# Performance work log

Hardware: AMD Instinct MI355X
Metric: run time of the kernel (lower is better)

The kernel has to match this reference:

```python
import jax, jax.numpy as jnp
import numpy as np

N_HEADS = 16
ROPE_BASE = 10000.0


def _rope_tables(T, head_dim, dtype):
    inv_freq = 1.0 / (ROPE_BASE ** (jnp.arange(0, head_dim, 2, dtype=jnp.float32) / head_dim))
    t = jnp.arange(T, dtype=jnp.float32)
    freqs = jnp.outer(t, inv_freq)              # (T, head_dim/2)
    emb = jnp.concatenate([freqs, freqs], -1)   # (T, head_dim)
    return jnp.cos(emb).astype(dtype), jnp.sin(emb).astype(dtype)


def _rotate_half(x):
    x1, x2 = jnp.split(x, 2, axis=-1)
    return jnp.concatenate([-x2, x1], axis=-1)


def setup_inputs() -> dict:
    key = jax.random.key(0)
    k1, k2, k3 = jax.random.split(key, 3)
    B, T, C = 2, 2048, 2048
    x = jax.random.normal(k1, (B, T, C), dtype=jnp.float32)
    Wqkv = jax.random.normal(k2, (C, 3 * C), dtype=jnp.float32) * (1.0 / np.sqrt(C))
    Wproj = jax.random.normal(k3, (C, C), dtype=jnp.float32) * (1.0 / np.sqrt(C))
    return {"x": x, "Wqkv": Wqkv, "Wproj": Wproj}


def reference(x, Wqkv, Wproj):
    B, T, C = x.shape
    H = N_HEADS
    D = C // H
    qkv = jnp.einsum('btc,cd->btd', x, Wqkv)            # (B,T,3C)
    q, k, v = jnp.split(qkv, 3, axis=-1)
    # (B,T,C) -> (B,H,T,D)
    q = q.reshape(B, T, H, D).transpose(0, 2, 1, 3)
    k = k.reshape(B, T, H, D).transpose(0, 2, 1, 3)
    v = v.reshape(B, T, H, D).transpose(0, 2, 1, 3)
    cos, sin = _rope_tables(T, D, x.dtype)              # (T,D) each
    q = q * cos + _rotate_half(q) * sin
    k = k * cos + _rotate_half(k) * sin
    scale = 1.0 / jnp.sqrt(jnp.asarray(D, x.dtype))
    att = jnp.einsum('bhqd,bhkd->bhqk', q, k) * scale   # (B,H,T,T)
    causal = jnp.tril(jnp.ones((T, T), dtype=bool))
    att = jnp.where(causal, att, jnp.asarray(-jnp.inf, att.dtype))
    att = jax.nn.softmax(att, axis=-1)
    y = jnp.einsum('bhqk,bhkd->bhqd', att, v)           # (B,H,T,D)
    y = y.transpose(0, 2, 1, 3).reshape(B, T, C)
    return jnp.einsum('btc,cd->btd', y, Wproj)
```

## Files before the change

kernel.cpp:

```cpp
#include <hip/hip_runtime.h>
#include <stdint.h>

#define T_SEQ 2048
#define NH 16
#define HD 128
#define CC 2048
#define N3 6144
#define MM 4096

typedef short bf16x8 __attribute__((ext_vector_type(8)));
typedef float f32x4 __attribute__((ext_vector_type(4)));

__device__ __forceinline__ unsigned short f2bf(float f) {
  unsigned int u = __float_as_uint(f);
  u += 0x7FFF + ((u >> 16) & 1);
  return (unsigned short)(u >> 16);
}
__device__ __forceinline__ float bf2f(unsigned short h) {
  return __uint_as_float(((unsigned int)h) << 16);
}

__global__ __launch_bounds__(256) void k_transpose_cvt(const float* __restrict__ in,
                                                       unsigned short* __restrict__ out,
                                                       int K, int N) {
  __shared__ float tile[32][33];
  int k0 = blockIdx.x * 32;
  int n0 = blockIdx.y * 32;
  int tx = threadIdx.x & 31, ty = threadIdx.x >> 5;
  #pragma unroll
  for (int r = ty; r < 32; r += 8)
    tile[r][tx] = in[(size_t)(k0 + r) * N + n0 + tx];
  __syncthreads();
  #pragma unroll
  for (int r = ty; r < 32; r += 8)
    out[(size_t)(n0 + r) * K + k0 + tx] = f2bf(tile[tx][r]);
}

__global__ __launch_bounds__(256) void k_cvt(const float* __restrict__ in,
                                             unsigned short* __restrict__ out, int n4) {
  int i = blockIdx.x * 256 + threadIdx.x;
  if (i >= n4) return;
  float4 v = ((const float4*)in)[i];
  ushort4 o;
  o.x = f2bf(v.x); o.y = f2bf(v.y); o.z = f2bf(v.z); o.w = f2bf(v.w);
  ((ushort4*)out)[i] = o;
}

template<int NJ, int EPI, int MMAJ>
__global__ __launch_bounds__(512, 1) void k_gemm8(const unsigned short* __restrict__ A,
                                                  const unsigned short* __restrict__ Bt,
                                                  float* __restrict__ C,
                                                  unsigned short* __restrict__ qo,
                                                  unsigned short* __restrict__ ko,
                                                  unsigned short* __restrict__ vo,
                                                  int M, int N, int K) {
  constexpr int BU = NJ / 2;
  constexpr int DSTRIDE = (1 + BU) * 16384;
  extern __shared__ __align__(16) char lds[];
  const int tid = threadIdx.x;
  const int lane = tid & 63;
  const int lr = lane & 15, lg = lane >> 4;
  const int wave = tid >> 6;
  const int wm = wave >> 2, wn = wave & 3;
  const int nwg = gridDim.x;
  const int bid = blockIdx.x;
  const int wg = (bid & 7) * (nwg >> 3) + (bid >> 3);
  const int GX = M >> 7;
  const int GN = N / (NJ * 64);
  const int mt = MMAJ ? (wg % GX) : (wg / GN);
  const int nt = MMAJ ? (wg / GX) : (wg % GN);
  const int m0 = mt * 128, n0 = nt * NJ * 64;
  const int NT = K >> 6;

  auto STAGE = [&](int d, int op, int h, int t) {
    const unsigned short* src = op ? Bt : A;
    const int r0 = (op ? n0 + h * 128 : m0);
    const int kc = t * 64;
    char* base = lds + d * DSTRIDE + op * 16384 + h * 16384;
    #pragma unroll
    for (int l = 0; l < 2; ++l) {
      int p = (l * 512 + tid) * 16;
      int qq = p ^ (((p >> 7) & 7) << 4);
      const unsigned short* g = src + (size_t)(r0 + (qq >> 7)) * K + kc + ((qq & 127) >> 1);
      __builtin_amdgcn_global_load_lds(
          (const __attribute__((address_space(1))) void*)g,
          (__attribute__((address_space(3))) void*)(base + (l * 512 + (tid & 448)) * 16),
          16, 0, 0);
    }
  };
  auto RD = [&](int d, int op, int row, int kb) -> bf16x8 {
    const char* base = lds + d * DSTRIDE + op * 16384;
    int p = row * 128 + kb;
    p ^= ((p >> 7) & 7) << 4;
    return *(const bf16x8*)(base + p);
  };

  f32x4 acc[4][NJ];
  #pragma unroll
  for (int i = 0; i < 4; ++i)
    #pragma unroll
    for (int j = 0; j < NJ; ++j) acc[i][j] = (f32x4){0.f, 0.f, 0.f, 0.f};

  bf16x8 bfrg[NJ][2];

#define PHASE(D, MI, READB, DOST, SD, SO, SH, ST, VM)                                    \
  {                                                                                      \
    if (READB) {                                                                         \
      _Pragma("unroll")                                                                  \
      for (int nj = 0; nj < NJ; ++nj)                                                    \
        _Pragma("unroll")                                                                \
        for (int ks = 0; ks < 2; ++ks)                                                   \
          bfrg[nj][ks] = RD(D, 1, wn * NJ * 16 + nj * 16 + lr, ks * 64 + lg * 16);       \
    }                                                                                    \
    bf16x8 af[2];                                                                        \
    _Pragma("unroll")                                                                    \
    for (int ks = 0; ks < 2; ++ks)                                                       \
      af[ks] = RD(D, 0, wm * 64 + (MI) * 16 + lr, ks * 64 + lg * 16);                    \
    if (DOST) STAGE(SD, SO, SH, ST);                                                     \
    __builtin_amdgcn_s_barrier();                                                        \
    asm volatile("s_waitcnt lgkmcnt(0)" ::: "memory");                                   \
    __builtin_amdgcn_s_setprio(1);                                                       \
    _Pragma("unroll")                                                                    \
    for (int nj = 0; nj < NJ; ++nj)                                                      \
      _Pragma("unroll")                                                                  \
      for (int ks = 0; ks < 2; ++ks)                                                     \
        acc[MI][nj] = __builtin_amdgcn_mfma_f32_16x16x32_bf16(af[ks], bfrg[nj][ks], acc[MI][nj], 0, 0, 0); \
    __builtin_amdgcn_s_setprio(0);                                                       \
    if ((VM) == 6) asm volatile("s_waitcnt vmcnt(6)" ::: "memory");                      \
    if ((VM) == 4) asm volatile("s_waitcnt vmcnt(4)" ::: "memory");                      \
    __builtin_amdgcn_s_barrier();                                                        \
  }

  const int t1 = NT > 1 ? 1 : 0;
  #pragma unroll
  for (int h = 0; h < BU; ++h) STAGE(0, 1, h, 0);
  STAGE(0, 0, 0, 0);
  #pragma unroll
  for (int h = 0; h < BU; ++h) STAGE(1, 1, h, t1);
  if (NJ == 6) asm volatile("s_waitcnt vmcnt(6)" ::: "memory");
  else         asm volatile("s_waitcnt vmcnt(4)" ::: "memory");
  __builtin_amdgcn_s_barrier();

  for (int it = 0; it < (NT >> 1); ++it) {
    const int tb  = 2 * it + 1;
    const int ta1 = min(2 * it + 2, NT - 1);
    const int tb1 = min(2 * it + 3, NT - 1);
    if (NJ == 6) {
      PHASE(0, 0, true,  true, 1, 0, 0, tb,  -1)
      PHASE(0, 1, false, true, 0, 1, 0, ta1, -1)
      PHASE(0, 2, false, true, 0, 1, 1, ta1, -1)
      PHASE(0, 3, false, true, 0, 1, 2, ta1,  6)
      PHASE(1, 0, true,  true, 0, 0, 0, ta1, -1)
      PHASE(1, 1, false, true, 1, 1, 0, tb1, -1)
      PHASE(1, 2, false, true, 1, 1, 1, tb1, -1)
      PHASE(1, 3, false, true, 1, 1, 2, tb1,  6)
    } else {
      PHASE(0, 0, true,  true,  1, 0, 0, tb,  -1)
      PHASE(0, 1, false, true,  0, 1, 0, ta1, -1)
      PHASE(0, 2, false, true,  0, 1, 1, ta1, -1)
      PHASE(0, 3, false, false, 0, 0, 0, 0,    4)
      PHASE(1, 0, true,  true,  0, 0, 0, ta1, -1)
      PHASE(1, 1, false, true,  1, 1, 0, tb1, -1)
      PHASE(1, 2, false, true,  1, 1, 1, tb1, -1)
      PHASE(1, 3, false, false, 0, 0, 0, 0,    4)
    }
  }
#undef PHASE

  #pragma unroll
  for (int mi = 0; mi < 4; ++mi) {
    #pragma unroll
    for (int nj = 0; nj < NJ; ++nj) {
      #pragma unroll
      for (int j = 0; j < 4; ++j) {
        int m = m0 + wm * 64 + mi * 16 + lg * 4 + j;
        int n = n0 + wn * NJ * 16 + nj * 16 + lr;
        float val = acc[mi][nj][j];
        if (EPI == 0) {
          C[(size_t)m * N + n] = val;
        } else {
          int which = n >> 11, cc = n & 2047;
          int h = cc >> 7, d = cc & 127;
          int b = m >> 11, t = m & 2047;
          unsigned short* dst = which == 0 ? qo : (which == 1 ? ko : vo);
          dst[(((size_t)(b * NH + h)) * T_SEQ + t) * HD + d] = f2bf(val);
        }
      }
    }
  }
}

__global__ __launch_bounds__(256) void k_rope(unsigned short* __restrict__ q,
                                              unsigned short* __restrict__ k) {
  int i = blockIdx.x * 256 + threadIdx.x;
  int d = i & 63;
  int t = (i >> 6) & (T_SEQ - 1);
  int bh = i >> 17;
  float invf = exp2f((float)(-2 * d) * (13.287712379549449f / 128.f));
  float ang = (float)t * invf;
  float c = cosf(ang), s = sinf(ang);
  size_t base = ((size_t)bh * T_SEQ + t) * HD + d;
  const float scale = 0.08838834764831845f;
  float q1 = bf2f(q[base]), q2 = bf2f(q[base + 64]);
  q[base]      = f2bf((q1 * c - q2 * s) * scale);
  q[base + 64] = f2bf((q2 * c + q1 * s) * scale);
  float k1 = bf2f(k[base]), k2 = bf2f(k[base + 64]);
  k[base]      = f2bf(k1 * c - k2 * s);
  k[base + 64] = f2bf(k2 * c + k1 * s);
}

__global__ __launch_bounds__(256) void k_transpose_v(const unsigned short* __restrict__ in,
                                                     unsigned short* __restrict__ out) {
  __shared__ unsigned short tile[32][33];
  int bh = blockIdx.z;
  int t0 = blockIdx.x * 32, d0 = blockIdx.y * 32;
  int tx = threadIdx.x & 31, ty = threadIdx.x >> 5;
  const unsigned short* src = in + (size_t)bh * T_SEQ * HD;
  unsigned short* dst = out + (size_t)bh * HD * T_SEQ;
  #pragma unroll
  for (int r = ty; r < 32; r += 8)
    tile[r][tx] = src[(size_t)(t0 + r) * HD + d0 + tx];
  __syncthreads();
  #pragma unroll
  for (int r = ty; r < 32; r += 8)
    dst[(size_t)(d0 + r) * T_SEQ + t0 + tx] = tile[tx][r];
}

__global__ __launch_bounds__(512) void k_attn(const unsigned short* __restrict__ Q,
                                              const unsigned short* __restrict__ K,
                                              const unsigned short* __restrict__ Vt,
                                              unsigned short* __restrict__ Y) {
  __shared__ __align__(16) unsigned short Ks[64 * 128];
  __shared__ __align__(16) unsigned short Vs[128 * 64];
  __shared__ __align__(16) unsigned short Ps[128 * 80];
  const int id = blockIdx.x;
  const int sub = id & 255;
  const int bh = sub & 31;
  const int qtl = (id < 256) ? (15 - (sub >> 5)) : (sub >> 5);
  const int b = bh >> 4, h = bh & 15;
  const int tid = threadIdx.x, wave = tid >> 6, lane = tid & 63;
  const int lr = lane & 15, lg = lane >> 4;
  const int q0 = qtl * 128;
  const int jtmax = 2 * qtl + 1;
  const unsigned short* Qb = Q + (size_t)bh * T_SEQ * HD;
  const unsigned short* Kb = K + (size_t)bh * T_SEQ * HD;
  const unsigned short* Vb = Vt + (size_t)bh * HD * T_SEQ;

  int rkA[2], okA[2], rvA[2], ovA[2], bkA[2], bvA[2];
  #pragma unroll
  for (int it = 0; it < 2; ++it) {
    int c = it * 512 + tid;
    rkA[it] = c >> 4; okA[it] = (c & 15) * 8;
    bkA[it] = (rkA[it] * 256 + (c & 15) * 16) ^ ((rkA[it] & 7) << 4);
    rvA[it] = c >> 3; ovA[it] = (c & 7) * 8;
    bvA[it] = (rvA[it] * 128 + (c & 7) * 16) ^ ((rvA[it] & 7) << 4);
  }

  bf16x8 qf[4];
  #pragma unroll
  for (int kk = 0; kk < 4; ++kk)
    qf[kk] = *(const bf16x8*)(Qb + (size_t)(q0 + wave * 16 + lr) * HD + kk * 32 + lg * 8);

  const f32x4 fzero = {0.f, 0.f, 0.f, 0.f};
  f32x4 oacc[8];
  #pragma unroll
  for (int nd = 0; nd < 8; ++nd) oacc[nd] = fzero;
  float mrow[4], lrow[4];
  #pragma unroll
  for (int j = 0; j < 4; ++j) { mrow[j] = -1e30f; lrow[j] = 0.f; }

  bf16x8 kst[2], vst[2];
  #pragma unroll
  for (int it = 0; it < 2; ++it) {
    kst[it] = *(const bf16x8*)(Kb + (size_t)rkA[it] * HD + okA[it]);
    vst[it] = *(const bf16x8*)(Vb + (size_t)rvA[it] * T_SEQ + ovA[it]);
  }

  for (int jt = 0; jt <= jtmax; ++jt) {
    const int tk0 = jt * 64;
    __syncthreads();
    #pragma unroll
    for (int it = 0; it < 2; ++it) {
      *(bf16x8*)((char*)Ks + bkA[it]) = kst[it];
      *(bf16x8*)((char*)Vs + bvA[it]) = vst[it];
    }
    if (jt < jtmax) {
      const int nk0 = tk0 + 64;
      #pragma unroll
      for (int it = 0; it < 2; ++it) {
        kst[it] = *(const bf16x8*)(Kb + (size_t)(nk0 + rkA[it]) * HD + okA[it]);
        vst[it] = *(const bf16x8*)(Vb + (size_t)rvA[it] * T_SEQ + nk0 + ovA[it]);
      }
    }
    __syncthreads();

    f32x4 sacc[4];
    #pragma unroll
    for (int nr = 0; nr < 4; ++nr) sacc[nr] = fzero;
    #pragma unroll
    for (int nr = 0; nr < 4; ++nr) {
      #pragma unroll
      for (int kk = 0; kk < 4; ++kk) {
        int row = nr * 16 + lr;
        int byte = (row * 256 + kk * 64 + lg * 16) ^ ((row & 7) << 4);
        bf16x8 kf = *(const bf16x8*)((char*)Ks + byte);
        sacc[nr] = __builtin_amdgcn_mfma_f32_16x16x32_bf16(qf[kk], kf, sacc[nr], 0, 0, 0);
      }
    }

    if (jt >= 2 * qtl) {
      #pragma unroll
      for (int nr = 0; nr < 4; ++nr)
        #pragma unroll
        for (int j = 0; j < 4; ++j) {
          int qg = q0 + wave * 16 + lg * 4 + j;
          int cg = tk0 + nr * 16 + lr;
          if (cg > qg) sacc[nr][j] = -1e30f;
        }
    }

    float oscale[4];
    #pragma unroll
    for (int j = 0; j < 4; ++j) {
      float tmax = fmaxf(fmaxf(sacc[0][j], sacc[1][j]), fmaxf(sacc[2][j], sacc[3][j]));
      #pragma unroll
      for (int m = 1; m <= 8; m <<= 1) tmax = fmaxf(tmax, __shfl_xor(tmax, m));
      float mnew = fmaxf(mrow[j], tmax);
      oscale[j] = __expf(mrow[j] - mnew);
      float rsum = 0.f;
      #pragma unroll
      for (int nr = 0; nr < 4; ++nr) {
        float p = __expf(sacc[nr][j] - mnew);
        Ps[(wave * 16 + lg * 4 + j) * 80 + nr * 16 + lr] = f2bf(p);
        rsum += p;
      }
      #pragma unroll
      for (int m = 1; m <= 8; m <<= 1) rsum += __shfl_xor(rsum, m);
      lrow[j] = lrow[j] * oscale[j] + rsum;
      mrow[j] = mnew;
    }
    #pragma unroll
    for (int nd = 0; nd < 8; ++nd)
      #pragma unroll
      for (int j = 0; j < 4; ++j) oacc[nd][j] *= oscale[j];

    bf16x8 pf[2];
    #pragma unroll
    for (int kk = 0; kk < 2; ++kk)
      pf[kk] = *(const bf16x8*)(Ps + (wave * 16 + lr) * 80 + kk * 32 + lg * 8);
    #pragma unroll
    for (int nd = 0; nd < 8; ++nd) {
      #pragma unroll
      for (int kk = 0; kk < 2; ++kk) {
        int row = nd * 16 + lr;
        int byte = (row * 128 + kk * 64 + lg * 16) ^ ((row & 7) << 4);
        bf16x8 vf = *(const bf16x8*)((char*)Vs + byte);
        oacc[nd] = __builtin_amdgcn_mfma_f32_16x16x32_bf16(pf[kk], vf, oacc[nd], 0, 0, 0);
      }
    }
  }

  #pragma unroll
  for (int j = 0; j < 4; ++j) {
    float inv = 1.f / lrow[j];
    int qg = q0 + wave * 16 + lg * 4 + j;
    size_t base = ((size_t)b * T_SEQ + qg) * CC + h * HD;
    #pragma unroll
    for (int nd = 0; nd < 8; ++nd)
      Y[base + nd * 16 + lr] = f2bf(oacc[nd][j] * inv);
  }
}

extern "C" void kernel_launch(void* const* d_in, const int* in_sizes, int n_in,
                              void* d_out, int out_size, void* d_ws, size_t ws_size,
                              hipStream_t stream) {
  const float* x     = (const float*)d_in[0];
  const float* Wqkv  = (const float*)d_in[1];
  const float* Wproj = (const float*)d_in[2];
  float* out = (float*)d_out;
  char* ws = (char*)d_ws;
  const size_t MB = 1024 * 1024;
  unsigned short* WqkvT  = (unsigned short*)(ws + 0);
  unsigned short* vt     = (unsigned short*)(ws + 0);
  unsigned short* WprojT = (unsigned short*)(ws + 24 * MB);
  unsigned short* xb     = (unsigned short*)(ws + 32 * MB);
  unsigned short* y      = xb;
  unsigned short* q      = (unsigned short*)(ws + 48 * MB);
  unsigned short* k      = (unsigned short*)(ws + 64 * MB);
  unsigned short* v      = (unsigned short*)(ws + 80 * MB);

  k_transpose_cvt<<<dim3(CC / 32, N3 / 32), 256, 0, stream>>>(Wqkv, WqkvT, CC, N3);
  k_transpose_cvt<<<dim3(CC / 32, CC / 32), 256, 0, stream>>>(Wproj, WprojT, CC, CC);
  k_cvt<<<(MM * CC / 4) / 256, 256, 0, stream>>>(x, xb, MM * CC / 4);
  k_gemm8<6, 1, 1><<<dim3((MM / 128) * (N3 / 384)), 512, 131072, stream>>>(
      xb, WqkvT, nullptr, q, k, v, MM, N3, CC);
  k_rope<<<(32 * T_SEQ * 64) / 256, 256, 0, stream>>>(q, k);
  k_transpose_v<<<dim3(T_SEQ / 32, HD / 32, 32), 256, 0, stream>>>(v, vt);
  k_attn<<<dim3(512), 512, 0, stream>>>(q, k, vt, y);
  k_gemm8<4, 0, 0><<<dim3((MM / 128) * (CC / 256)), 512, 98304, stream>>>(
      y, WprojT, out, nullptr, nullptr, nullptr, MM, CC, CC);
}
```

Baseline: 297.1 us.

## Process two 16-row query groups per wave in attention with half the waves

The attention kernel now runs 4 waves per block (256 threads) instead of 8. Each wave handles 32 query rows as two 16-row groups, so every K and V fragment read from shared memory feeds two MFMAs instead of one. The change also wraps the MFMA loops in s_setprio so the matrix-core phases get scheduling priority. The goal is fewer LDS reads per MFMA. The cost is more registers per wave (doubled accumulators and Q fragments), fewer waves to hide latency, and twice as many global load iterations per thread for staging K and V.

```diff
diff --git a/kernel.cpp b/kernel.cpp
--- a/kernel.cpp
+++ b/kernel.cpp
@@ -226,10 +226,10 @@
     dst[(size_t)(d0 + r) * T_SEQ + t0 + tx] = tile[tx][r];
 }
 
-__global__ __launch_bounds__(512) void k_attn(const unsigned short* __restrict__ Q,
-                                              const unsigned short* __restrict__ K,
-                                              const unsigned short* __restrict__ Vt,
-                                              unsigned short* __restrict__ Y) {
+__global__ __launch_bounds__(256, 2) void k_attn(const unsigned short* __restrict__ Q,
+                                                 const unsigned short* __restrict__ K,
+                                                 const unsigned short* __restrict__ Vt,
+                                                 unsigned short* __restrict__ Y) {
   __shared__ __align__(16) unsigned short Ks[64 * 128];
   __shared__ __align__(16) unsigned short Vs[128 * 64];
   __shared__ __align__(16) unsigned short Ps[128 * 80];
@@ -246,32 +246,38 @@
   const unsigned short* Kb = K + (size_t)bh * T_SEQ * HD;
   const unsigned short* Vb = Vt + (size_t)bh * HD * T_SEQ;
 
-  int rkA[2], okA[2], rvA[2], ovA[2], bkA[2], bvA[2];
-  #pragma unroll
-  for (int it = 0; it < 2; ++it) {
-    int c = it * 512 + tid;
+  int rkA[4], okA[4], rvA[4], ovA[4], bkA[4], bvA[4];
+  #pragma unroll
+  for (int it = 0; it < 4; ++it) {
+    int c = it * 256 + tid;
     rkA[it] = c >> 4; okA[it] = (c & 15) * 8;
     bkA[it] = (rkA[it] * 256 + (c & 15) * 16) ^ ((rkA[it] & 7) << 4);
     rvA[it] = c >> 3; ovA[it] = (c & 7) * 8;
     bvA[it] = (rvA[it] * 128 + (c & 7) * 16) ^ ((rvA[it] & 7) << 4);
   }
 
-  bf16x8 qf[4];
-  #pragma unroll
-  for (int kk = 0; kk < 4; ++kk)
-    qf[kk] = *(const bf16x8*)(Qb + (size_t)(q0 + wave * 16 + lr) * HD + kk * 32 + lg * 8);
+  bf16x8 qf[2][4];
+  #pragma unroll
+  for (int g = 0; g < 2; ++g)
+    #pragma unroll
+    for (int kk = 0; kk < 4; ++kk)
+      qf[g][kk] = *(const bf16x8*)(Qb + (size_t)(q0 + wave * 32 + g * 16 + lr) * HD + kk * 32 + lg * 8);
 
   const f32x4 fzero = {0.f, 0.f, 0.f, 0.f};
-  f32x4 oacc[8];
-  #pragma unroll
-  for (int nd = 0; nd < 8; ++nd) oacc[nd] = fzero;
-  float mrow[4], lrow[4];
-  #pragma unroll
-  for (int j = 0; j < 4; ++j) { mrow[j] = -1e30f; lrow[j] = 0.f; }
-
-  bf16x8 kst[2], vst[2];
-  #pragma unroll
-  for (int it = 0; it < 2; ++it) {
+  f32x4 oacc[2][8];
+  #pragma unroll
+  for (int g = 0; g < 2; ++g)
+    #pragma unroll
+    for (int nd = 0; nd < 8; ++nd) oacc[g][nd] = fzero;
+  float mrow[2][4], lrow[2][4];
+  #pragma unroll
+  for (int g = 0; g < 2; ++g)
+    #pragma unroll
+    for (int j = 0; j < 4; ++j) { mrow[g][j] = -1e30f; lrow[g][j] = 0.f; }
+
+  bf16x8 kst[4], vst[4];
+  #pragma unroll
+  for (int it = 0; it < 4; ++it) {
     kst[it] = *(const bf16x8*)(Kb + (size_t)rkA[it] * HD + okA[it]);
     vst[it] = *(const bf16x8*)(Vb + (size_t)rvA[it] * T_SEQ + ovA[it]);
   }
@@ -280,23 +286,26 @@
     const int tk0 = jt * 64;
     __syncthreads();
     #pragma unroll
-    for (int it = 0; it < 2; ++it) {
+    for (int it = 0; it < 4; ++it) {
       *(bf16x8*)((char*)Ks + bkA[it]) = kst[it];
       *(bf16x8*)((char*)Vs + bvA[it]) = vst[it];
     }
     if (jt < jtmax) {
       const int nk0 = tk0 + 64;
       #pragma unroll
-      for (int it = 0; it < 2; ++it) {
+      for (int it = 0; it < 4; ++it) {
         kst[it] = *(const bf16x8*)(Kb + (size_t)(nk0 + rkA[it]) * HD + okA[it]);
         vst[it] = *(const bf16x8*)(Vb + (size_t)rvA[it] * T_SEQ + nk0 + ovA[it]);
       }
     }
     __syncthreads();
 
-    f32x4 sacc[4];
-    #pragma unroll
-    for (int nr = 0; nr < 4; ++nr) sacc[nr] = fzero;
+    f32x4 sacc[2][4];
+    #pragma unroll
+    for (int g = 0; g < 2; ++g)
+      #pragma unroll
+      for (int nr = 0; nr < 4; ++nr) sacc[g][nr] = fzero;
+    __builtin_amdgcn_s_setprio(1);
     #pragma unroll
     for (int nr = 0; nr < 4; ++nr) {
       #pragma unroll
@@ -304,50 +313,60 @@
         int row = nr * 16 + lr;
         int byte = (row * 256 + kk * 64 + lg * 16) ^ ((row & 7) << 4);
         bf16x8 kf = *(const bf16x8*)((char*)Ks + byte);
-        sacc[nr] = __builtin_amdgcn_mfma_f32_16x16x32_bf16(qf[kk], kf, sacc[nr], 0, 0, 0);
+        sacc[0][nr] = __builtin_amdgcn_mfma_f32_16x16x32_bf16(qf[0][kk], kf, sacc[0][nr], 0, 0, 0);
+        sacc[1][nr] = __builtin_amdgcn_mfma_f32_16x16x32_bf16(qf[1][kk], kf, sacc[1][nr], 0, 0, 0);
       }
     }
+    __builtin_amdgcn_s_setprio(0);
 
     if (jt >= 2 * qtl) {
       #pragma unroll
-      for (int nr = 0; nr < 4; ++nr)
+      for (int g = 0; g < 2; ++g)
         #pragma unroll
-        for (int j = 0; j < 4; ++j) {
-          int qg = q0 + wave * 16 + lg * 4 + j;
-          int cg = tk0 + nr * 16 + lr;
-          if (cg > qg) sacc[nr][j] = -1e30f;
+        for (int nr = 0; nr < 4; ++nr)
+          #pragma unroll
+          for (int j = 0; j < 4; ++j) {
+            int qg = q0 + wave * 32 + g * 16 + lg * 4 + j;
+            int cg = tk0 + nr * 16 + lr;
+            if (cg > qg) sacc[g][nr][j] = -1e30f;
+          }
+    }
+
+    #pragma unroll
+    for (int g = 0; g < 2; ++g) {
+      float oscale[4];
+      #pragma unroll
+      for (int j = 0; j < 4; ++j) {
+        float tmax = fmaxf(fmaxf(sacc[g][0][j], sacc[g][1][j]), fmaxf(sacc[g][2][j], sacc[g][3][j]));
+        #pragma unroll
+        for (int m = 1; m <= 8; m <<= 1) tmax = fmaxf(tmax, __shfl_xor(tmax, m));
+        float mnew = fmaxf(mrow[g][j], tmax);
+        oscale[j] = __expf(mrow[g][j] - mnew);
+        float rsum = 0.f;
+        #pragma unroll
+        for (int nr = 0; nr < 4; ++nr) {
+          float p = __expf(sacc[g][nr][j] - mnew);
+          Ps[(wave * 32 + g * 16 + lg * 4 + j) * 80 + nr * 16 + lr] = f2bf(p);
+          rsum += p;
         }
-    }
-
-    float oscale[4];
-    #pragma unroll
-    for (int j = 0; j < 4; ++j) {
-      float tmax = fmaxf(fmaxf(sacc[0][j], sacc[1][j]), fmaxf(sacc[2][j], sacc[3][j]));
-      #pragma unroll
-      for (int m = 1; m <= 8; m <<= 1) tmax = fmaxf(tmax, __shfl_xor(tmax, m));
-      float mnew = fmaxf(mrow[j], tmax);
-      oscale[j] = __expf(mrow[j] - mnew);
-      float rsum = 0.f;
-      #pragma unroll
-      for (int nr = 0; nr < 4; ++nr) {
-        float p = __expf(sacc[nr][j] - mnew);
-        Ps[(wave * 16 + lg * 4 + j) * 80 + nr * 16 + lr] = f2bf(p);
-        rsum += p;
+        #pragma unroll
+        for (int m = 1; m <= 8; m <<= 1) rsum += __shfl_xor(rsum, m);
+        lrow[g][j] = lrow[g][j] * oscale[j] + rsum;
+        mrow[g][j] = mnew;
       }
       #pragma unroll
-      for (int m = 1; m <= 8; m <<= 1) rsum += __shfl_xor(rsum, m);
-      lrow[j] = lrow[j] * oscale[j] + rsum;
-      mrow[j] = mnew;
-    }
-    #pragma unroll
-    for (int nd = 0; nd < 8; ++nd)
-      #pragma unroll
-      for (int j = 0; j < 4; ++j) oacc[nd][j] *= oscale[j];
-
-    bf16x8 pf[2];
-    #pragma unroll
-    for (int kk = 0; kk < 2; ++kk)
-      pf[kk] = *(const bf16x8*)(Ps + (wave * 16 + lr) * 80 + kk * 32 + lg * 8);
+      for (int nd = 0; nd < 8; ++nd)
+        #pragma unroll
+        for (int j = 0; j < 4; ++j) oacc[g][nd][j] *= oscale[j];
+    }
+
+    bf16x8 pf[2][2];
+    #pragma unroll
+    for (int g = 0; g < 2; ++g)
+      #pragma unroll
+      for (int kk = 0; kk < 2; ++kk)
+        pf[g][kk] = *(const bf16x8*)(Ps + (wave * 32 + g * 16 + lr) * 80 + kk * 32 + lg * 8);
+    __builtin_amdgcn_s_setprio(1);
     #pragma unroll
     for (int nd = 0; nd < 8; ++nd) {
       #pragma unroll
@@ -355,20 +374,24 @@
         int row = nd * 16 + lr;
         int byte = (row * 128 + kk * 64 + lg * 16) ^ ((row & 7) << 4);
         bf16x8 vf = *(const bf16x8*)((char*)Vs + byte);
-        oacc[nd] = __builtin_amdgcn_mfma_f32_16x16x32_bf16(pf[kk], vf, oacc[nd], 0, 0, 0);
+        oacc[0][nd] = __builtin_amdgcn_mfma_f32_16x16x32_bf16(pf[0][kk], vf, oacc[0][nd], 0, 0, 0);
+        oacc[1][nd] = __builtin_amdgcn_mfma_f32_16x16x32_bf16(pf[1][kk], vf, oacc[1][nd], 0, 0, 0);
       }
     }
-  }
-
-  #pragma unroll
-  for (int j = 0; j < 4; ++j) {
-    float inv = 1.f / lrow[j];
-    int qg = q0 + wave * 16 + lg * 4 + j;
-    size_t base = ((size_t)b * T_SEQ + qg) * CC + h * HD;
-    #pragma unroll
-    for (int nd = 0; nd < 8; ++nd)
-      Y[base + nd * 16 + lr] = f2bf(oacc[nd][j] * inv);
-  }
+    __builtin_amdgcn_s_setprio(0);
+  }
+
+  #pragma unroll
+  for (int g = 0; g < 2; ++g)
+    #pragma unroll
+    for (int j = 0; j < 4; ++j) {
+      float inv = 1.f / lrow[g][j];
+      int qg = q0 + wave * 32 + g * 16 + lg * 4 + j;
+      size_t base = ((size_t)b * T_SEQ + qg) * CC + h * HD;
+      #pragma unroll
+      for (int nd = 0; nd < 8; ++nd)
+        Y[base + nd * 16 + lr] = f2bf(oacc[g][nd][j] * inv);
+    }
 }
 
 extern "C" void kernel_launch(void* const* d_in, const int* in_sizes, int n_in,
@@ -396,7 +419,7 @@
       xb, WqkvT, nullptr, q, k, v, MM, N3, CC);
   k_rope<<<(32 * T_SEQ * 64) / 256, 256, 0, stream>>>(q, k);
   k_transpose_v<<<dim3(T_SEQ / 32, HD / 32, 32), 256, 0, stream>>>(v, vt);
-  k_attn<<<dim3(512), 512, 0, stream>>>(q, k, vt, y);
+  k_attn<<<dim3(512), 256, 0, stream>>>(q, k, vt, y);
   k_gemm8<4, 0, 0><<<dim3((MM / 128) * (CC / 256)), 512, 98304, stream>>>(
       y, WprojT, out, nullptr, nullptr, nullptr, MM, CC, CC);
 }
```

Measured after the change: 304.0 us. 1.02x slower.
